# Kernel optimization log

Hardware: AMD Instinct MI355X
Metric: run time of the kernel (lower is better)

Reference implementation:

```python
import jax, jax.numpy as jnp
import numpy as np

N_NODES = 50000
N_EDGES = 800000
IN_DIM = 128
OUT_DIM = 64
K_KERNELS = 2
S_ATTEN = 2


def setup_inputs() -> dict:
    key = jax.random.key(0)
    ks = jax.random.split(key, 9)
    return {
        "x": jax.random.normal(ks[0], (N_NODES, IN_DIM), dtype=jnp.float32),
        "support_vals": jax.random.uniform(ks[1], (K_KERNELS, N_EDGES), dtype=jnp.float32),
        "atten_vals": jax.random.uniform(ks[2], (S_ATTEN, N_EDGES), dtype=jnp.float32),
        "W_transform": jax.random.normal(ks[3], (K_KERNELS, IN_DIM, OUT_DIM), dtype=jnp.float32) * 0.05,
        "w_left": jax.random.normal(ks[4], (K_KERNELS, S_ATTEN + 1, OUT_DIM), dtype=jnp.float32) * 0.05,
        "w_right": jax.random.normal(ks[5], (K_KERNELS, S_ATTEN + 1, OUT_DIM), dtype=jnp.float32) * 0.05,
        "W_residual": jax.random.normal(ks[6], (IN_DIM + OUT_DIM, OUT_DIM), dtype=jnp.float32) * 0.05,
        "edge_rows": jax.random.randint(ks[7], (N_EDGES,), 0, N_NODES, dtype=jnp.int64),
        "edge_cols": jax.random.randint(ks[8], (N_EDGES,), 0, N_NODES, dtype=jnp.int64),
    }


def reference(x, support_vals, atten_vals, W_transform, w_left, w_right, W_residual, edge_rows, edge_cols):
    # x: [N, F], edge lists: [E]; all supports share the same sparsity pattern.
    N = x.shape[0]
    K = W_transform.shape[0]
    output = jnp.zeros((N, W_transform.shape[2]), dtype=x.dtype)
    for k in range(K):
        wx = x @ W_transform[k]                       # [N, D]
        al = wx @ w_left[k].T                         # [N, S+1]
        ar = wx @ w_right[k].T                        # [N, S+1]
        # per-support edge values; support i=S uses this kernel's Cheb support
        vals = jnp.concatenate([atten_vals, support_vals[k][None, :]], axis=0)  # [S+1, E]
        # score_e = sum_i (al[row_e,i] + ar[col_e,i]) * vals[i,e]
        scores = jnp.einsum('es,se->e', al[edge_rows] + ar[edge_cols], vals)    # [E]
        # row-wise (segment) softmax over nonzeros, as tf.sparse_softmax
        m = jax.ops.segment_max(scores, edge_rows, num_segments=N)              # [N]
        ex = jnp.exp(scores - m[edge_rows])
        denom = jax.ops.segment_sum(ex, edge_rows, num_segments=N)              # [N]
        probs = ex / denom[edge_rows]                                           # [E]
        # spmm: out[r] = sum_{e: row_e=r} probs_e * wx[col_e]
        output = output + jax.ops.segment_sum(probs[:, None] * wx[edge_cols], edge_rows, num_segments=N)
    # residual projection then elu activation
    output = jnp.concatenate([x, output], axis=-1) @ W_residual
    return jax.nn.elu(output)
```

## Files before the change

### kernel.cpp

```cpp
#include <hip/hip_runtime.h>

#define N_NODES 50000
#define N_EDGES 800000
#define IN_DIM 128
#define OUT_DIM 64
#define NEG_INF (-1e30f)
#define GBLK ((N_NODES + 63) / 64)
#define BSHIFT 6
#define NBUK ((N_NODES + 63) >> 6)
#define NBUKP 784
#define EB 1024
#define PREB ((N_EDGES + EB - 1) / EB)
#define NFRAG (3 * 16 + 8)
#define STAGE_CAP 2048
#define BUKCAP 2048

typedef unsigned short ushort_t;
typedef __attribute__((ext_vector_type(8))) short short8;
typedef __attribute__((ext_vector_type(4))) float f32x4;
typedef __attribute__((ext_vector_type(2))) _Float16 half2_t;

__device__ __forceinline__ unsigned f2bf(float f) {
    unsigned u = __float_as_uint(f);
    u += 0x7fffu + ((u >> 16) & 1u);
    return u >> 16;
}
__device__ __forceinline__ float bf2f(ushort_t h) {
    return __uint_as_float((unsigned)h << 16);
}
__device__ __forceinline__ unsigned rl_u(unsigned v, int i) {
    return __builtin_amdgcn_readlane(v, i);
}
__device__ __forceinline__ unsigned pack_h2(float a, float b) {
    auto h = __builtin_amdgcn_cvt_pkrtz(a, b);
    union { decltype(h) h2; unsigned u; } v; v.h2 = h; return v.u;
}
__device__ __forceinline__ void unpack_h2(unsigned u, float& a, float& b) {
    union { unsigned u; half2_t h; } v; v.u = u;
    a = (float)v.h[0];
    b = (float)v.h[1];
}
__device__ __forceinline__ float dot2u(unsigned w, unsigned p, float acc) {
    union { unsigned u; half2_t h; } wv, pv;
    wv.u = w; pv.u = p;
    return __builtin_amdgcn_fdot2(wv.h, pv.h, acc, false);
}

__global__ void wpack_kernel(const float* __restrict__ Wt,
                             const float* __restrict__ Wres,
                             ushort_t* __restrict__ Wpack) {
    int idx = blockIdx.x * 256 + threadIdx.x;
    if (idx >= NFRAG * 512) return;
    int f = idx >> 9;
    int within = idx & 511;
    int lane = within >> 3;
    int b = within & 7;
    float val;
    if (f < 48) {
        int mat = f >> 4;
        int ct = (f >> 2) & 3;
        int kc = f & 3;
        int k = kc * 32 + (lane >> 4) * 8 + b;
        int c = ct * 16 + (lane & 15);
        const float* W = (mat < 2) ? (Wt + (size_t)mat * IN_DIM * OUT_DIM) : Wres;
        val = W[(size_t)k * OUT_DIM + c];
    } else {
        int f2 = f - 48;
        int ct = f2 >> 1;
        int kc = f2 & 1;
        int k = kc * 32 + (lane >> 4) * 8 + b;
        int c = ct * 16 + (lane & 15);
        val = Wres[(size_t)(IN_DIM + k) * OUT_DIM + c];
    }
    Wpack[idx] = (ushort_t)f2bf(val);
}

__global__ __launch_bounds__(256) void gemm_kernel(
        const float* __restrict__ x,
        const ushort_t* __restrict__ Wpack,
        const float* __restrict__ wl,
        const float* __restrict__ wr,
        unsigned* __restrict__ wxi,
        ushort_t* __restrict__ xresh,
        float* __restrict__ al,
        float* __restrict__ ar) {
    int wave = threadIdx.x >> 6;
    int lane = threadIdx.x & 63;
    int lr = lane & 15;
    int lg = lane >> 4;
    int row0 = blockIdx.x * 64 + wave * 16;

    int arow = row0 + lr;
    if (arow >= N_NODES) arow = N_NODES - 1;
    const float* xr = x + (size_t)arow * IN_DIM;
    short8 afrag[4];
#pragma unroll
    for (int kc = 0; kc < 4; ++kc) {
        float4 f0 = *(const float4*)(xr + kc * 32 + lg * 8);
        float4 f1 = *(const float4*)(xr + kc * 32 + lg * 8 + 4);
        short8 a;
        a[0] = (short)f2bf(f0.x); a[1] = (short)f2bf(f0.y);
        a[2] = (short)f2bf(f0.z); a[3] = (short)f2bf(f0.w);
        a[4] = (short)f2bf(f1.x); a[5] = (short)f2bf(f1.y);
        a[6] = (short)f2bf(f1.z); a[7] = (short)f2bf(f1.w);
        afrag[kc] = a;
    }

    f32x4 acc[3][4] = {};
#pragma unroll
    for (int kc = 0; kc < 4; ++kc) {
#pragma unroll
        for (int mat = 0; mat < 3; ++mat) {
#pragma unroll
            for (int ct = 0; ct < 4; ++ct) {
                short8 bfrag = *(const short8*)(
                    Wpack + (size_t)(((mat * 4 + ct) * 4 + kc) << 9) + lane * 8);
                acc[mat][ct] = __builtin_amdgcn_mfma_f32_16x16x32_bf16(
                    afrag[kc], bfrag, acc[mat][ct], 0, 0, 0);
            }
        }
    }

#pragma unroll
    for (int r = 0; r < 4; ++r) {
        int gr = row0 + lg * 4 + r;
        if (gr < N_NODES) {
#pragma unroll
            for (int ct = 0; ct < 4; ++ct) {
                wxi[(size_t)gr * OUT_DIM + ct * 16 + lr] =
                    pack_h2(acc[0][ct][r], acc[1][ct][r]);
                xresh[(size_t)gr * OUT_DIM + ct * 16 + lr] =
                    (ushort_t)f2bf(acc[2][ct][r]);
            }
        }
    }

#pragma unroll
    for (int mat = 0; mat < 2; ++mat) {
#pragma unroll
        for (int s = 0; s < 3; ++s) {
            float wlv[4], wrv[4];
#pragma unroll
            for (int ct = 0; ct < 4; ++ct) {
                wlv[ct] = wl[(size_t)(mat * 3 + s) * OUT_DIM + ct * 16 + lr];
                wrv[ct] = wr[(size_t)(mat * 3 + s) * OUT_DIM + ct * 16 + lr];
            }
#pragma unroll
            for (int r = 0; r < 4; ++r) {
                float pl = 0.f, pr = 0.f;
#pragma unroll
                for (int ct = 0; ct < 4; ++ct) {
                    pl = fmaf(acc[mat][ct][r], wlv[ct], pl);
                    pr = fmaf(acc[mat][ct][r], wrv[ct], pr);
                }
#pragma unroll
                for (int off = 1; off < 16; off <<= 1) {
                    pl += __shfl_xor(pl, off);
                    pr += __shfl_xor(pr, off);
                }
                if (lr == 0) {
                    int gr = row0 + lg * 4 + r;
                    if (gr < N_NODES) {
                        al[(size_t)gr * 6 + mat * 3 + s] = pl;
                        ar[(size_t)gr * 6 + mat * 3 + s] = pr;
                    }
                }
            }
        }
    }
}

__global__ __launch_bounds__(256) void score_sort_kernel(
        const int* __restrict__ rows,
        const int* __restrict__ cols,
        const float* __restrict__ atten,
        const float* __restrict__ support,
        const float* __restrict__ al,
        const float* __restrict__ ar,
        uint2* __restrict__ etmp,
        uint2* __restrict__ cl) {
    __shared__ int cnt[1024];
    __shared__ int cur[1024];
    __shared__ int aux[256];
    __shared__ uint2 stage[EB];
    int t = threadIdx.x;
    cnt[t] = 0; cnt[t + 256] = 0; cnt[t + 512] = 0; cnt[t + 768] = 0;
    __syncthreads();
    int base0 = blockIdx.x * EB;
    int nval = min(EB, N_EDGES - base0);

    int r_[4], c_[4];
    float s0_[4], s1_[4];
#pragma unroll
    for (int i = 0; i < 4; ++i) {
        int e = base0 + i * 256 + t;
        bool v = e < N_EDGES;
        int r = v ? rows[e] : -1;
        int c = v ? cols[e] : 0;
        float sc0 = 0.f, sc1 = 0.f;
        if (v) {
            float a0 = atten[e], a1 = atten[N_EDGES + e];
            float sp0 = support[e], sp1 = support[N_EDGES + e];
            const float* A = al + (size_t)r * 6;
            const float* B = ar + (size_t)c * 6;
            sc0 = (A[0] + B[0]) * a0 + (A[1] + B[1]) * a1 + (A[2] + B[2]) * sp0;
            sc1 = (A[3] + B[3]) * a0 + (A[4] + B[4]) * a1 + (A[5] + B[5]) * sp1;
            atomicAdd(&cnt[r >> BSHIFT], 1);
        }
        r_[i] = r; c_[i] = c; s0_[i] = sc0; s1_[i] = sc1;
    }
    __syncthreads();
    int v0 = cnt[4 * t], v1 = cnt[4 * t + 1], v2 = cnt[4 * t + 2], v3 = cnt[4 * t + 3];
    int ps = v0 + v1 + v2 + v3;
    aux[t] = ps;
    __syncthreads();
    int val = ps;
    for (int off = 1; off < 256; off <<= 1) {
        int y = (t >= off) ? aux[t - off] : 0;
        __syncthreads();
        val += y; aux[t] = val;
        __syncthreads();
    }
    int e0x = val - ps;
    cur[4 * t]     = e0x;
    cur[4 * t + 1] = e0x + v0;
    cur[4 * t + 2] = e0x + v0 + v1;
    cur[4 * t + 3] = e0x + v0 + v1 + v2;
    size_t cb = (size_t)blockIdx.x * NBUKP;
    int vv[4] = {v0, v1, v2, v3};
#pragma unroll
    for (int j = 0; j < 4; ++j) {
        int idx = 4 * t + j;
        if (idx < NBUK) cl[cb + idx] = make_uint2((unsigned)vv[j], (unsigned)cur[idx]);
    }
    __syncthreads();
#pragma unroll
    for (int i = 0; i < 4; ++i) {
        if (r_[i] < 0) continue;
        int pos = atomicAdd(&cur[r_[i] >> BSHIFT], 1);
        uint2 pv;
        pv.x = (unsigned)c_[i] | ((unsigned)(r_[i] & 63) << 16);
        pv.y = pack_h2(s0_[i], s1_[i]);
        stage[pos] = pv;
    }
    __syncthreads();
    for (int i = t; i < nval; i += 256)
        etmp[(size_t)base0 + i] = stage[i];
}

__global__ __launch_bounds__(256) void sortb_kernel(
        const uint2* __restrict__ cl,
        const uint2* __restrict__ etmp,
        uint2* __restrict__ edata,
        uint2* __restrict__ rowinfo) {
    __shared__ uint2 stage[STAGE_CAP];
    __shared__ int rpos[PREB + 2];
    __shared__ int lloff[PREB];
    __shared__ int aux[256];
    __shared__ int hist[64], rcur[64];
    int k = blockIdx.x, t = threadIdx.x;
    int base = k * BUKCAP;

    for (int b = t; b < PREB; b += 256) {
        uint2 v2 = cl[(size_t)b * NBUKP + k];
        rpos[b] = (int)v2.x;
        lloff[b] = (int)v2.y;
    }
    if (t < 64) hist[t] = 0;
    __syncthreads();
    int v[4];
    int idx4 = 4 * t;
#pragma unroll
    for (int i = 0; i < 4; ++i) v[i] = (idx4 + i < PREB) ? rpos[idx4 + i] : 0;
    __syncthreads();
    int s = 0;
#pragma unroll
    for (int i = 0; i < 4; ++i) { int tmp = v[i]; v[i] = s; s += tmp; }
    aux[t] = s;
    __syncthreads();
    int tv = s;
    for (int off = 1; off < 256; off <<= 1) {
        int y = (t >= off) ? aux[t - off] : 0;
        __syncthreads();
        tv += y; aux[t] = tv;
        __syncthreads();
    }
    int ofs = tv - s;
#pragma unroll
    for (int i = 0; i < 4; ++i)
        if (idx4 + i <= PREB) rpos[idx4 + i] = ofs + v[i];
    __syncthreads();
    int nb = rpos[PREB];

    for (int b = t; b < PREB; b += 256) {
        int s0 = rpos[b];
        int n = rpos[b + 1] - s0;
        int lo = lloff[b];
        const uint2* src = etmp + (size_t)b * EB + lo;
        for (int i = 0; i < n; ++i) {
            uint2 rec = src[i];
            int j = s0 + i;
            if (j < STAGE_CAP) stage[j] = rec;
            atomicAdd(&hist[(rec.x >> 16) & 63], 1);
        }
    }
    __syncthreads();
    int hv = (t < 64) ? hist[t] : 0;
    aux[t] = hv;
    __syncthreads();
    int hval = hv;
    for (int off = 1; off < 64; off <<= 1) {
        int y = (t >= off && t < 64) ? aux[t - off] : 0;
        __syncthreads();
        hval += y; aux[t] = hval;
        __syncthreads();
    }
    if (t < 64) {
        int start = hval - hv;
        rcur[t] = start;
        int row = (k << BSHIFT) + t;
        if (row < N_NODES)
            rowinfo[row] = make_uint2((unsigned)(base + start), (unsigned)hv);
    }
    __syncthreads();
    for (int j = t; j < nb; j += 256) {
        uint2 rec;
        if (j < STAGE_CAP) rec = stage[j];
        else {
            int lo = 0, hi = PREB - 1;
            while (lo < hi) { int mid = (lo + hi + 1) >> 1; if (rpos[mid] <= j) lo = mid; else hi = mid - 1; }
            rec = etmp[(size_t)lo * EB + lloff[lo] + (j - rpos[lo])];
        }
        int rl = (rec.x >> 16) & 63;
        int dst = atomicAdd(&rcur[rl], 1);
        if (dst < BUKCAP) edata[(size_t)base + dst] = rec;
    }
}

__global__ __launch_bounds__(256) void attn_resid_kernel(
        const uint2* __restrict__ rowinfo,
        const uint2* __restrict__ edata,
        const unsigned* __restrict__ wxi,
        const ushort_t* __restrict__ xresh,
        const ushort_t* __restrict__ Wpack,
        float* __restrict__ out) {
    __shared__ ushort_t aacc_s[64][72];
    int t = threadIdx.x;
    int wave = t >> 6;
    int lane = t & 63;
    for (int i = t; i < 64 * 36; i += 256) ((unsigned*)aacc_s)[i] = 0;
    __syncthreads();

    for (int rr = wave; rr < 64; rr += 4) {
        int row = blockIdx.x * 64 + rr;
        if (row >= N_NODES) continue;
        uint2 ri = rowinfo[row];
        int beg = (int)ri.x;
        int deg = (int)ri.y;
        float a = 0.f;

        if (deg > 0 && deg <= 64) {
            bool valid = lane < deg;
            uint2 ed = edata[valid ? beg + lane : beg];
            unsigned c = ed.x & 0xFFFFu;
            float sc0, sc1;
            unpack_h2(ed.y, sc0, sc1);
            if (!valid) { sc0 = NEG_INF; sc1 = NEG_INF; }
            float m0 = sc0, m1 = sc1;
#pragma unroll
            for (int off = 32; off > 0; off >>= 1) {
                m0 = fmaxf(m0, __shfl_xor(m0, off));
                m1 = fmaxf(m1, __shfl_xor(m1, off));
            }
            float e0 = valid ? __expf(sc0 - m0) : 0.f;
            float e1 = valid ? __expf(sc1 - m1) : 0.f;
            float l0 = e0, l1 = e1;
#pragma unroll
            for (int off = 32; off > 0; off >>= 1) {
                l0 += __shfl_xor(l0, off);
                l1 += __shfl_xor(l1, off);
            }
            unsigned pp = pack_h2(e0 / l0, e1 / l1);
            float acc8[8] = {};
            int i = 0;
            for (; i + 8 <= deg; i += 8) {
                unsigned cc[8], vv8[8];
#pragma unroll
                for (int j = 0; j < 8; ++j) cc[j] = rl_u(c, i + j);
#pragma unroll
                for (int j = 0; j < 8; ++j) vv8[j] = wxi[(size_t)cc[j] * OUT_DIM + lane];
#pragma unroll
                for (int j = 0; j < 8; ++j)
                    acc8[j] = dot2u(vv8[j], rl_u(pp, i + j), acc8[j]);
            }
            for (; i < deg; ++i) {
                unsigned ci = rl_u(c, i);
                unsigned vw = wxi[(size_t)ci * OUT_DIM + lane];
                acc8[0] = dot2u(vw, rl_u(pp, i), acc8[0]);
            }
            a = ((acc8[0] + acc8[1]) + (acc8[2] + acc8[3]))
              + ((acc8[4] + acc8[5]) + (acc8[6] + acc8[7]));
        } else if (deg > 64) {
            int end = beg + deg;
            float m0 = NEG_INF, l0 = 0.f, m1 = NEG_INF, l1 = 0.f;
            for (int base = beg; base < end; base += 64) {
                int pos = base + lane;
                bool valid = pos < end;
                uint2 ed = edata[valid ? pos : beg];
                float sc0, sc1;
                unpack_h2(ed.y, sc0, sc1);
                if (!valid) { sc0 = NEG_INF; sc1 = NEG_INF; }
                float cm0 = sc0, cm1 = sc1;
#pragma unroll
                for (int off = 32; off > 0; off >>= 1) {
                    cm0 = fmaxf(cm0, __shfl_xor(cm0, off));
                    cm1 = fmaxf(cm1, __shfl_xor(cm1, off));
                }
                float mn0 = fmaxf(m0, cm0), mn1 = fmaxf(m1, cm1);
                float e0 = valid ? __expf(sc0 - mn0) : 0.f;
                float e1 = valid ? __expf(sc1 - mn1) : 0.f;
#pragma unroll
                for (int off = 32; off > 0; off >>= 1) {
                    e0 += __shfl_xor(e0, off);
                    e1 += __shfl_xor(e1, off);
                }
                l0 = l0 * __expf(m0 - mn0) + e0;
                l1 = l1 * __expf(m1 - mn1) + e1;
                m0 = mn0; m1 = mn1;
            }
            float inv0 = 1.f / l0, inv1 = 1.f / l1;
            for (int base = beg; base < end; base += 64) {
                int pos = base + lane;
                bool valid = pos < end;
                uint2 ed = edata[valid ? pos : beg];
                unsigned c = ed.x & 0xFFFFu;
                float sc0, sc1;
                unpack_h2(ed.y, sc0, sc1);
                float p0 = valid ? __expf(sc0 - m0) * inv0 : 0.f;
                float p1 = valid ? __expf(sc1 - m1) * inv1 : 0.f;
                unsigned pp = pack_h2(p0, p1);
                int cnt = min(64, end - base);
                for (int i = 0; i < cnt; ++i) {
                    unsigned ci = rl_u(c, i);
                    unsigned vw = wxi[(size_t)ci * OUT_DIM + lane];
                    a = dot2u(vw, rl_u(pp, i), a);
                }
            }
        }
        aacc_s[rr][lane] = (ushort_t)f2bf(a);
    }
    __syncthreads();

    int lr = lane & 15;
    int lg = lane >> 4;
    int row0 = blockIdx.x * 64 + wave * 16;
    int rloc = wave * 16 + lr;
    short8 af[2];
#pragma unroll
    for (int kc = 0; kc < 2; ++kc)
        af[kc] = *(const short8*)&aacc_s[rloc][kc * 32 + lg * 8];
    f32x4 acc4[4] = {};
#pragma unroll
    for (int kc = 0; kc < 2; ++kc) {
#pragma unroll
        for (int ct = 0; ct < 4; ++ct) {
            short8 bfrag = *(const short8*)(
                Wpack + (size_t)((48 + ct * 2 + kc) << 9) + lane * 8);
            acc4[ct] = __builtin_amdgcn_mfma_f32_16x16x32_bf16(
                af[kc], bfrag, acc4[ct], 0, 0, 0);
        }
    }
#pragma unroll
    for (int r = 0; r < 4; ++r) {
        int gr = row0 + lg * 4 + r;
        if (gr < N_NODES) {
#pragma unroll
            for (int ct = 0; ct < 4; ++ct) {
                float v = acc4[ct][r] + bf2f(xresh[(size_t)gr * OUT_DIM + ct * 16 + lr]);
                out[(size_t)gr * OUT_DIM + ct * 16 + lr] = (v > 0.f) ? v : expm1f(v);
            }
        }
    }
}

extern "C" void kernel_launch(void* const* d_in, const int* in_sizes, int n_in,
                              void* d_out, int out_size, void* d_ws, size_t ws_size,
                              hipStream_t stream) {
    const float* x       = (const float*)d_in[0];
    const float* support = (const float*)d_in[1];
    const float* atten   = (const float*)d_in[2];
    const float* Wt      = (const float*)d_in[3];
    const float* wl      = (const float*)d_in[4];
    const float* wr      = (const float*)d_in[5];
    const float* Wres    = (const float*)d_in[6];
    const int*   rows    = (const int*)d_in[7];
    const int*   cols    = (const int*)d_in[8];
    float* out = (float*)d_out;

    unsigned* wxi    = (unsigned*)d_ws;
    ushort_t* xresh  = (ushort_t*)(wxi + (size_t)N_NODES * OUT_DIM);
    float* al        = (float*)(xresh + (size_t)N_NODES * OUT_DIM);
    float* ar        = al + (size_t)N_NODES * 6;
    uint2* etmp      = (uint2*)(ar + (size_t)N_NODES * 6);
    uint2* edata     = etmp + (size_t)N_EDGES;
    uint2* rowinfo   = edata + (size_t)NBUK * BUKCAP;
    uint2* cl        = rowinfo + N_NODES + 4;
    ushort_t* Wpack  = (ushort_t*)(cl + (size_t)PREB * NBUKP);

    wpack_kernel<<<(NFRAG * 512 + 255) / 256, 256, 0, stream>>>(Wt, Wres, Wpack);
    gemm_kernel<<<GBLK, 256, 0, stream>>>(x, Wpack, wl, wr, wxi, xresh, al, ar);
    score_sort_kernel<<<PREB, 256, 0, stream>>>(
        rows, cols, atten, support, al, ar, etmp, cl);
    sortb_kernel<<<NBUK, 256, 0, stream>>>(cl, etmp, edata, rowinfo);
    attn_resid_kernel<<<NBUK, 256, 0, stream>>>(
        rowinfo, edata, wxi, xresh, Wpack, out);
}
```

Baseline: 144.9 us.

## Split fused attention+residual kernel into per-row attention and separate MFMA residual kernel

Replaces the fused kernel, which had each wave process 16 rows serially before a shared-memory MFMA residual, with two kernels. The first launches one wave per node (12500 blocks) and writes bf16 aggregates to global memory, reusing the etmp buffer. The second reads those aggregates and runs the MFMA residual projection plus ELU. The aim is better load balance and more memory-level parallelism in the gather. The cost is an extra launch and a global round trip of the aggregates.

```diff
diff --git a/kernel.cpp b/kernel.cpp
--- a/kernel.cpp
+++ b/kernel.cpp
@@ -337,128 +337,126 @@
     }
 }
 
-__global__ __launch_bounds__(256) void attn_resid_kernel(
-        const uint2* __restrict__ rowinfo,
-        const uint2* __restrict__ edata,
-        const unsigned* __restrict__ wxi,
+__global__ void attn_kernel(const uint2* __restrict__ rowinfo,
+                            const uint2* __restrict__ edata,
+                            const unsigned* __restrict__ wxi,
+                            ushort_t* __restrict__ aacc) {
+    int wid = blockIdx.x * 4 + (threadIdx.x >> 6);
+    if (wid >= N_NODES) return;
+    int lane = threadIdx.x & 63;
+    uint2 ri = rowinfo[wid];
+    int beg = (int)ri.x;
+    int deg = (int)ri.y;
+    float a = 0.f;
+
+    if (deg > 0 && deg <= 64) {
+        bool valid = lane < deg;
+        uint2 ed = edata[valid ? beg + lane : beg];
+        unsigned c = ed.x & 0xFFFFu;
+        float sc0, sc1;
+        unpack_h2(ed.y, sc0, sc1);
+        if (!valid) { sc0 = NEG_INF; sc1 = NEG_INF; }
+        float m0 = sc0, m1 = sc1;
+#pragma unroll
+        for (int off = 32; off > 0; off >>= 1) {
+            m0 = fmaxf(m0, __shfl_xor(m0, off));
+            m1 = fmaxf(m1, __shfl_xor(m1, off));
+        }
+        float e0 = valid ? __expf(sc0 - m0) : 0.f;
+        float e1 = valid ? __expf(sc1 - m1) : 0.f;
+        float l0 = e0, l1 = e1;
+#pragma unroll
+        for (int off = 32; off > 0; off >>= 1) {
+            l0 += __shfl_xor(l0, off);
+            l1 += __shfl_xor(l1, off);
+        }
+        unsigned pp = pack_h2(e0 / l0, e1 / l1);
+        float acc8[8] = {};
+        int i = 0;
+        for (; i + 8 <= deg; i += 8) {
+            unsigned cc[8], vv[8];
+#pragma unroll
+            for (int j = 0; j < 8; ++j) cc[j] = rl_u(c, i + j);
+#pragma unroll
+            for (int j = 0; j < 8; ++j) vv[j] = wxi[(size_t)cc[j] * OUT_DIM + lane];
+#pragma unroll
+            for (int j = 0; j < 8; ++j)
+                acc8[j] = dot2u(vv[j], rl_u(pp, i + j), acc8[j]);
+        }
+        for (; i < deg; ++i) {
+            unsigned ci = rl_u(c, i);
+            unsigned v = wxi[(size_t)ci * OUT_DIM + lane];
+            acc8[0] = dot2u(v, rl_u(pp, i), acc8[0]);
+        }
+        a = ((acc8[0] + acc8[1]) + (acc8[2] + acc8[3]))
+          + ((acc8[4] + acc8[5]) + (acc8[6] + acc8[7]));
+    } else if (deg > 64) {
+        int end = beg + deg;
+        float m0 = NEG_INF, l0 = 0.f, m1 = NEG_INF, l1 = 0.f;
+        for (int base = beg; base < end; base += 64) {
+            int pos = base + lane;
+            bool valid = pos < end;
+            uint2 ed = edata[valid ? pos : beg];
+            float sc0, sc1;
+            unpack_h2(ed.y, sc0, sc1);
+            if (!valid) { sc0 = NEG_INF; sc1 = NEG_INF; }
+            float cm0 = sc0, cm1 = sc1;
+#pragma unroll
+            for (int off = 32; off > 0; off >>= 1) {
+                cm0 = fmaxf(cm0, __shfl_xor(cm0, off));
+                cm1 = fmaxf(cm1, __shfl_xor(cm1, off));
+            }
+            float mn0 = fmaxf(m0, cm0), mn1 = fmaxf(m1, cm1);
+            float e0 = valid ? __expf(sc0 - mn0) : 0.f;
+            float e1 = valid ? __expf(sc1 - mn1) : 0.f;
+#pragma unroll
+            for (int off = 32; off > 0; off >>= 1) {
+                e0 += __shfl_xor(e0, off);
+                e1 += __shfl_xor(e1, off);
+            }
+            l0 = l0 * __expf(m0 - mn0) + e0;
+            l1 = l1 * __expf(m1 - mn1) + e1;
+            m0 = mn0; m1 = mn1;
+        }
+        float inv0 = 1.f / l0, inv1 = 1.f / l1;
+        for (int base = beg; base < end; base += 64) {
+            int pos = base + lane;
+            bool valid = pos < end;
+            uint2 ed = edata[valid ? pos : beg];
+            unsigned c = ed.x & 0xFFFFu;
+            float sc0, sc1;
+            unpack_h2(ed.y, sc0, sc1);
+            float p0 = valid ? __expf(sc0 - m0) * inv0 : 0.f;
+            float p1 = valid ? __expf(sc1 - m1) * inv1 : 0.f;
+            unsigned pp = pack_h2(p0, p1);
+            int cnt = min(64, end - base);
+            for (int i = 0; i < cnt; ++i) {
+                unsigned ci = rl_u(c, i);
+                unsigned v = wxi[(size_t)ci * OUT_DIM + lane];
+                a = dot2u(v, rl_u(pp, i), a);
+            }
+        }
+    }
+    aacc[(size_t)wid * OUT_DIM + lane] = (ushort_t)f2bf(a);
+}
+
+__global__ __launch_bounds__(256) void resid_kernel(
+        const ushort_t* __restrict__ aacc,
         const ushort_t* __restrict__ xresh,
         const ushort_t* __restrict__ Wpack,
         float* __restrict__ out) {
-    __shared__ ushort_t aacc_s[64][72];
-    int t = threadIdx.x;
-    int wave = t >> 6;
-    int lane = t & 63;
-    for (int i = t; i < 64 * 36; i += 256) ((unsigned*)aacc_s)[i] = 0;
-    __syncthreads();
-
-    for (int rr = wave; rr < 64; rr += 4) {
-        int row = blockIdx.x * 64 + rr;
-        if (row >= N_NODES) continue;
-        uint2 ri = rowinfo[row];
-        int beg = (int)ri.x;
-        int deg = (int)ri.y;
-        float a = 0.f;
-
-        if (deg > 0 && deg <= 64) {
-            bool valid = lane < deg;
-            uint2 ed = edata[valid ? beg + lane : beg];
-            unsigned c = ed.x & 0xFFFFu;
-            float sc0, sc1;
-            unpack_h2(ed.y, sc0, sc1);
-            if (!valid) { sc0 = NEG_INF; sc1 = NEG_INF; }
-            float m0 = sc0, m1 = sc1;
-#pragma unroll
-            for (int off = 32; off > 0; off >>= 1) {
-                m0 = fmaxf(m0, __shfl_xor(m0, off));
-                m1 = fmaxf(m1, __shfl_xor(m1, off));
-            }
-            float e0 = valid ? __expf(sc0 - m0) : 0.f;
-            float e1 = valid ? __expf(sc1 - m1) : 0.f;
-            float l0 = e0, l1 = e1;
-#pragma unroll
-            for (int off = 32; off > 0; off >>= 1) {
-                l0 += __shfl_xor(l0, off);
-                l1 += __shfl_xor(l1, off);
-            }
-            unsigned pp = pack_h2(e0 / l0, e1 / l1);
-            float acc8[8] = {};
-            int i = 0;
-            for (; i + 8 <= deg; i += 8) {
-                unsigned cc[8], vv8[8];
-#pragma unroll
-                for (int j = 0; j < 8; ++j) cc[j] = rl_u(c, i + j);
-#pragma unroll
-                for (int j = 0; j < 8; ++j) vv8[j] = wxi[(size_t)cc[j] * OUT_DIM + lane];
-#pragma unroll
-                for (int j = 0; j < 8; ++j)
-                    acc8[j] = dot2u(vv8[j], rl_u(pp, i + j), acc8[j]);
-            }
-            for (; i < deg; ++i) {
-                unsigned ci = rl_u(c, i);
-                unsigned vw = wxi[(size_t)ci * OUT_DIM + lane];
-                acc8[0] = dot2u(vw, rl_u(pp, i), acc8[0]);
-            }
-            a = ((acc8[0] + acc8[1]) + (acc8[2] + acc8[3]))
-              + ((acc8[4] + acc8[5]) + (acc8[6] + acc8[7]));
-        } else if (deg > 64) {
-            int end = beg + deg;
-            float m0 = NEG_INF, l0 = 0.f, m1 = NEG_INF, l1 = 0.f;
-            for (int base = beg; base < end; base += 64) {
-                int pos = base + lane;
-                bool valid = pos < end;
-                uint2 ed = edata[valid ? pos : beg];
-                float sc0, sc1;
-                unpack_h2(ed.y, sc0, sc1);
-                if (!valid) { sc0 = NEG_INF; sc1 = NEG_INF; }
-                float cm0 = sc0, cm1 = sc1;
-#pragma unroll
-                for (int off = 32; off > 0; off >>= 1) {
-                    cm0 = fmaxf(cm0, __shfl_xor(cm0, off));
-                    cm1 = fmaxf(cm1, __shfl_xor(cm1, off));
-                }
-                float mn0 = fmaxf(m0, cm0), mn1 = fmaxf(m1, cm1);
-                float e0 = valid ? __expf(sc0 - mn0) : 0.f;
-                float e1 = valid ? __expf(sc1 - mn1) : 0.f;
-#pragma unroll
-                for (int off = 32; off > 0; off >>= 1) {
-                    e0 += __shfl_xor(e0, off);
-                    e1 += __shfl_xor(e1, off);
-                }
-                l0 = l0 * __expf(m0 - mn0) + e0;
-                l1 = l1 * __expf(m1 - mn1) + e1;
-                m0 = mn0; m1 = mn1;
-            }
-            float inv0 = 1.f / l0, inv1 = 1.f / l1;
-            for (int base = beg; base < end; base += 64) {
-                int pos = base + lane;
-                bool valid = pos < end;
-                uint2 ed = edata[valid ? pos : beg];
-                unsigned c = ed.x & 0xFFFFu;
-                float sc0, sc1;
-                unpack_h2(ed.y, sc0, sc1);
-                float p0 = valid ? __expf(sc0 - m0) * inv0 : 0.f;
-                float p1 = valid ? __expf(sc1 - m1) * inv1 : 0.f;
-                unsigned pp = pack_h2(p0, p1);
-                int cnt = min(64, end - base);
-                for (int i = 0; i < cnt; ++i) {
-                    unsigned ci = rl_u(c, i);
-                    unsigned vw = wxi[(size_t)ci * OUT_DIM + lane];
-                    a = dot2u(vw, rl_u(pp, i), a);
-                }
-            }
-        }
-        aacc_s[rr][lane] = (ushort_t)f2bf(a);
-    }
-    __syncthreads();
-
+    int wave = threadIdx.x >> 6;
+    int lane = threadIdx.x & 63;
     int lr = lane & 15;
     int lg = lane >> 4;
     int row0 = blockIdx.x * 64 + wave * 16;
-    int rloc = wave * 16 + lr;
+    int arow = row0 + lr;
+    if (arow >= N_NODES) arow = N_NODES - 1;
+    const ushort_t* ap = aacc + (size_t)arow * OUT_DIM;
     short8 af[2];
 #pragma unroll
     for (int kc = 0; kc < 2; ++kc)
-        af[kc] = *(const short8*)&aacc_s[rloc][kc * 32 + lg * 8];
+        af[kc] = *(const short8*)(ap + kc * 32 + lg * 8);
     f32x4 acc4[4] = {};
 #pragma unroll
     for (int kc = 0; kc < 2; ++kc) {
@@ -506,12 +504,14 @@
     uint2* rowinfo   = edata + (size_t)NBUK * BUKCAP;
     uint2* cl        = rowinfo + N_NODES + 4;
     ushort_t* Wpack  = (ushort_t*)(cl + (size_t)PREB * NBUKP);
+    ushort_t* aacc   = (ushort_t*)etmp;
 
     wpack_kernel<<<(NFRAG * 512 + 255) / 256, 256, 0, stream>>>(Wt, Wres, Wpack);
     gemm_kernel<<<GBLK, 256, 0, stream>>>(x, Wpack, wl, wr, wxi, xresh, al, ar);
     score_sort_kernel<<<PREB, 256, 0, stream>>>(
         rows, cols, atten, support, al, ar, etmp, cl);
     sortb_kernel<<<NBUK, 256, 0, stream>>>(cl, etmp, edata, rowinfo);
-    attn_resid_kernel<<<NBUK, 256, 0, stream>>>(
-        rowinfo, edata, wxi, xresh, Wpack, out);
-}
+    attn_kernel<<<(N_NODES + 3) / 4, 256, 0, stream>>>(
+        rowinfo, edata, wxi, aacc);
+    resid_kernel<<<GBLK, 256, 0, stream>>>(aacc, xresh, Wpack, out);
+}
```

After: 123.2 us. -15.0%, faster.
